# Kernel optimization log

Hardware: AMD Instinct MI355X
Metric: run time of the kernel (lower is better)

The kernel has to match this reference:

```python
import jax, jax.numpy as jnp
import numpy as np

N = 50000       # nodes
E = 800000      # directed edges
F_IN = 128      # input feature dim
HID = 128       # hidden channels
DEPTH = 3


def glorot(key, shape):
    lim = (6.0 / (shape[0] + shape[-1])) ** 0.5
    return jax.random.uniform(key, shape, jnp.float32, -lim, lim)


def setup_inputs():
    key = jax.random.key(0)
    ks = jax.random.split(key, 20)
    inp = {
        "x": jax.random.normal(ks[0], (N, F_IN), jnp.float32),
        "edge_index": jax.random.randint(ks[1], (E, 2), 0, N),
        "y": jax.random.randint(ks[2], (N,), 0, 2),
    }
    dd = [(F_IN, HID), (HID, HID), (HID, HID), (HID, HID)]
    for i, (a, b) in enumerate(dd):
        inp[f"Wd{i}"] = glorot(ks[3 + i], (a, b))
        inp[f"bd{i}"] = jnp.zeros((b,), jnp.float32)
    for i in range(DEPTH):
        inp[f"Wp{i}"] = glorot(ks[7 + i], (2 * HID,))
        inp[f"bp{i}"] = jnp.zeros((), jnp.float32)
    du = [(2 * HID, HID), (2 * HID, HID), (2 * HID + F_IN, 1)]
    for i, (a, b) in enumerate(du):
        inp[f"Wu{i}"] = glorot(ks[10 + i], (a, b))
        inp[f"bu{i}"] = jnp.zeros((b,), jnp.float32)
    return inp


def gcn_conv(x, src, dst, ew, W, b):
    """GCNConv(improved=True): A_hat = A + 2I, symmetric normalization.
    ew masks invalid (deduped/padded) edges with 0."""
    n = x.shape[0]
    deg = 2.0 + jax.ops.segment_sum(ew, dst, num_segments=n)  # self-loop weight 2
    dinv = jax.lax.rsqrt(deg)
    xw = x @ W                                   # [n, out]
    norm = ew * dinv[src] * dinv[dst]            # [E]
    out = jax.ops.segment_sum(xw[src] * norm[:, None], dst, num_segments=n)
    out = out + (2.0 * dinv * dinv)[:, None] * xw  # self-loop contribution
    return out + b


def connected_components(src, dst, sel, n):
    """Weak CC over selected edges via min-label propagation + pointer jumping.
    Returns per-node label = min node index in its component."""
    s = jnp.where(sel, src, 0)  # masked edges become (0,0) self-loops
    d = jnp.where(sel, dst, 0)

    def body(state):
        lab, _ = state
        m = jnp.minimum(lab[s], lab[d])
        new = lab.at[s].min(m).at[d].min(m)
        new = new[new]
        new = new[new]
        return new, jnp.any(new != lab)

    lab, _ = jax.lax.while_loop(lambda st: st[1], body,
                                (jnp.arange(n), jnp.array(True)))
    return lab


def cluster_pool(x, src, dst, ew, Wp, bp):
    """ClusterPooling (eval mode): score edges, contract score>0.5 edges,
    merge components (sum of members scaled by mean intra-cluster edge score).
    Pooled graph keeps N slots; cluster ids are representative node indices."""
    n, hid = x.shape
    valid = (ew > 0) & (src != dst)
    s = jax.nn.sigmoid(x[src] @ Wp[:hid] + x[dst] @ Wp[hid:] + bp)  # [E]
    sel = valid & (s > 0.5)
    cluster = jax.lax.stop_gradient(connected_components(src, dst, sel, n))
    csrc = cluster[src]
    ssum = jax.ops.segment_sum(jnp.where(sel, s, 0.0), csrc, num_segments=n)
    scnt = jax.ops.segment_sum(sel.astype(x.dtype), csrc, num_segments=n)
    w = jnp.where(scnt > 0, ssum / jnp.maximum(scnt, 1.0), 1.0)  # singletons -> 1
    new_x = jax.ops.segment_sum(x, cluster, num_segments=n) * w[:, None]
    # remap edges to clusters, drop self-loops, coalesce duplicates (static shape)
    a = jnp.where(valid, cluster[src], n)
    b = jnp.where(valid, cluster[dst], n)
    loop = a == b
    a = jnp.where(loop, n, a)
    b = jnp.where(loop, n, b)
    order = jnp.lexsort((b, a))
    a, b = a[order], b[order]
    dup = jnp.concatenate([jnp.zeros((1,), bool),
                           (a[1:] == a[:-1]) & (b[1:] == b[:-1])])
    keep = (a < n) & (~dup)
    new_ew = keep.astype(x.dtype)
    a = jnp.where(keep, a, 0)
    b = jnp.where(keep, b, 0)
    return new_x, a, b, new_ew, (src, dst, ew, cluster)


def reference(x, edge_index, y,
              Wd0, bd0, Wd1, bd1, Wd2, bd2, Wd3, bd3,
              Wp0, bp0, Wp1, bp1, Wp2, bp2,
              Wu0, bu0, Wu1, bu1, Wu2, bu2):
    Wd = [Wd0, Wd1, Wd2, Wd3]; bd = [bd0, bd1, bd2, bd3]
    Wp = [Wp0, Wp1, Wp2]; bp = [bp0, bp1, bp2]
    Wu = [Wu0, Wu1, Wu2]; bu = [bu0, bu1, bu2]
    src = edge_index[:, 0]
    dst = edge_index[:, 1]
    ew = jnp.ones(src.shape[0], x.dtype)
    x_in = x
    memory, infos = [], []
    for i in range(DEPTH):
        x = jax.nn.relu(gcn_conv(x, src, dst, ew, Wd[i], bd[i]))
        memory.append(x)
        x, src, dst, ew, info = cluster_pool(x, src, dst, ew, Wp[i], bp[i])
        infos.append(info)
    memory[0] = jnp.concatenate([memory[0], x_in], axis=-1)
    x = gcn_conv(x, src, dst, ew, Wd[3], bd[3])
    for i in range(DEPTH):
        src, dst, ew, cluster = infos.pop()
        x = x[cluster]                                  # unpool
        x = jnp.concatenate([memory.pop(), x], axis=-1)  # skip connection
        x = gcn_conv(x, src, dst, ew, Wu[i], bu[i])
        if i < DEPTH - 1:
            x = jax.nn.relu(x)
    return jax.nn.sigmoid(x).ravel()
```

## Files before the change

### kernel.cpp

```cpp
#include <hip/hip_runtime.h>
#include <math.h>

#define NN 50000
#define EE 800000
#define HID 128
#define HSZ (1u<<21)
#define CC_ROUNDS 8
#define GN 196
#define WH 512
#define CH 128


static __device__ __forceinline__ float sigmoid_ref(float t) {
  if (t >= 0.f) { float e = expf(-t); return 1.f / (1.f + e); }
  float e = expf(t); return e / (1.f + e);
}

static __device__ __forceinline__ int edge_count(const int* cntp, int cnst) {
  return cntp ? *cntp : cnst;
}


__global__ void k_split_edges(const int* __restrict__ ei, int* __restrict__ s, int* __restrict__ d) {
  int T = gridDim.x*blockDim.x;
  for (int e = blockIdx.x*blockDim.x+threadIdx.x; e < EE; e += T) {
    s[e] = ei[2*e]; d[e] = ei[2*e+1];
  }
}

__global__ void k_degree(const int* __restrict__ eB, const int* cntp, int cnst, int* __restrict__ deg) {
  int n = edge_count(cntp, cnst);
  int T = gridDim.x*blockDim.x;
  for (int e = blockIdx.x*blockDim.x+threadIdx.x; e < n; e += T)
    atomicAdd(&deg[eB[e]], 1);
}

__global__ void k_scan1(const int* __restrict__ deg, int* __restrict__ rp, int* __restrict__ bsum) {
  __shared__ int sh[256];
  int tid = threadIdx.x; int i = blockIdx.x*256 + tid;
  int v = (i < NN) ? deg[i] : 0;
  sh[tid] = v; __syncthreads();
  for (int off = 1; off < 256; off <<= 1) {
    int t = (tid >= off) ? sh[tid-off] : 0;
    __syncthreads(); sh[tid] += t; __syncthreads();
  }
  if (i < NN) rp[i] = sh[tid] - v;
  if (tid == 255) bsum[blockIdx.x] = sh[255];
}

__global__ void k_scan2(int* __restrict__ bsum, int* __restrict__ rp, int nb) {
  __shared__ int sh[256];
  int tid = threadIdx.x;
  int v = (tid < nb) ? bsum[tid] : 0;
  sh[tid] = v; __syncthreads();
  for (int off = 1; off < 256; off <<= 1) {
    int t = (tid >= off) ? sh[tid-off] : 0;
    __syncthreads(); sh[tid] += t; __syncthreads();
  }
  if (tid < nb) bsum[tid] = sh[tid] - v;
  if (tid == 255) rp[NN] = sh[255];
}

__global__ void k_scan3(int* __restrict__ rp, const int* __restrict__ bsum, int* __restrict__ cursor,
                        const int* __restrict__ deg, float* __restrict__ dinv) {
  int i = blockIdx.x*256 + threadIdx.x;
  if (i < NN) {
    int r = rp[i] + bsum[blockIdx.x];
    rp[i] = r; cursor[i] = r;
    if (dinv) dinv[i] = (float)(1.0 / sqrt((double)(deg[i] + 2)));
  }
}

__global__ void k_csrfill(const int* __restrict__ eA, const int* __restrict__ eB,
                          const int* cntp, int cnst,
                          int* __restrict__ cursor, int* __restrict__ csr, int* __restrict__ dstE) {
  int n = edge_count(cntp, cnst);
  int T = gridDim.x*blockDim.x;
  for (int e = blockIdx.x*blockDim.x+threadIdx.x; e < n; e += T) {
    int d = eB[e];
    int p = atomicAdd(&cursor[d], 1);
    csr[p] = eA[e];
    dstE[p] = d;
  }
}


__global__ __launch_bounds__(256) void k_matmul(
    const float* __restrict__ A0, const int* __restrict__ idx0, int reluA0,
    const float* __restrict__ rsA, const float* __restrict__ rcA,
    const float* __restrict__ A1, const int* __restrict__ idx1, int reluA1,
    int K, const float* __restrict__ W, const float* __restrict__ dinv,
    const float* __restrict__ bias, float* __restrict__ xs, float* __restrict__ outi)
{
  __shared__ __align__(16) float As[64][68];
  __shared__ __align__(16) float Bs[64][HID];
  const int tid  = threadIdx.x;
  const int row0 = blockIdx.x * 64;
  const int colg = (tid & 31) * 4;
  const int rowg = (tid >> 5) * 8;
  float acc[8][4];
  #pragma unroll
  for (int i = 0; i < 8; ++i) { acc[i][0]=0.f; acc[i][1]=0.f; acc[i][2]=0.f; acc[i][3]=0.f; }

  for (int kc = 0; kc < K; kc += 64) {
    const bool first = (kc < 128);
    const float* Asrc = first ? A0 : A1;
    const int*   aidx = first ? idx0 : idx1;
    const int    relu = first ? reluA0 : reluA1;
    const int klocal  = first ? kc : (kc - 128);
    #pragma unroll
    for (int t = tid; t < 64*16; t += 256) {
      int r  = t >> 4;
      int k4 = (t & 15) << 2;
      int grow = row0 + r;
      if (grow >= NN) grow = NN - 1;
      int gr = aidx ? aidx[grow] : grow;
      float4 v = *(const float4*)(Asrc + (size_t)gr*HID + klocal + k4);
      if (relu) {
        v.x = fmaxf(v.x,0.f); v.y = fmaxf(v.y,0.f);
        v.z = fmaxf(v.z,0.f); v.w = fmaxf(v.w,0.f);
      }
      if (first && rsA) {
        float c = rcA[gr];
        float w = (c > 0.f) ? rsA[gr]/c : 1.f;
        v.x *= w; v.y *= w; v.z *= w; v.w *= w;
      }
      As[k4+0][r] = v.x; As[k4+1][r] = v.y; As[k4+2][r] = v.z; As[k4+3][r] = v.w;
    }
    #pragma unroll
    for (int t = tid; t < 64*32; t += 256) {
      int kk = t >> 5;
      int c4 = (t & 31) << 2;
      *(float4*)&Bs[kk][c4] = *(const float4*)(W + (size_t)(kc+kk)*HID + c4);
    }
    __syncthreads();
    #pragma unroll 8
    for (int k = 0; k < 64; ++k) {
      float4 a0 = *(const float4*)&As[k][rowg];
      float4 a1 = *(const float4*)&As[k][rowg+4];
      float4 b  = *(const float4*)&Bs[k][colg];
      float ar[8] = {a0.x,a0.y,a0.z,a0.w,a1.x,a1.y,a1.z,a1.w};
      #pragma unroll
      for (int i = 0; i < 8; ++i) {
        acc[i][0] += ar[i]*b.x; acc[i][1] += ar[i]*b.y;
        acc[i][2] += ar[i]*b.z; acc[i][3] += ar[i]*b.w;
      }
    }
    __syncthreads();
  }
  float4 bb = *(const float4*)(bias + colg);
  #pragma unroll
  for (int i = 0; i < 8; ++i) {
    int r = row0 + rowg + i;
    if (r < NN) {
      float dv = dinv[r];
      float4 xv = make_float4(acc[i][0]*dv, acc[i][1]*dv, acc[i][2]*dv, acc[i][3]*dv);
      *(float4*)(xs + (size_t)r*HID + colg) = xv;
      float c2 = 2.f*dv;
      *(float4*)(outi + (size_t)r*HID + colg) =
        make_float4(xv.x*c2+bb.x, xv.y*c2+bb.y, xv.z*c2+bb.z, xv.w*c2+bb.w);
    }
  }
}

__global__ __launch_bounds__(256) void k_edgeagg(
    const float* __restrict__ xs, const int* __restrict__ csr, const int* __restrict__ dstE,
    const float* __restrict__ dinv, float* __restrict__ out,
    const int* cntp, int cnst)
{
  __shared__ int sh_s[8][CH];
  __shared__ int sh_d[8][CH];
  int n = edge_count(cntp, cnst);
  const int lane = threadIdx.x & 31;
  const int gsub = threadIdx.x >> 5;
  const int grp  = blockIdx.x*8 + gsub;
  const int p0   = grp * CH;
  if (p0 >= n) return;
  const int cnt = min(CH, n - p0);

  for (int j = lane; j < cnt; j += 32) {
    sh_s[gsub][j] = csr[p0 + j];
    sh_d[gsub][j] = dstE[p0 + j];
  }

  float4 pf[4];
  #pragma unroll
  for (int j = 0; j < 4; ++j) {
    if (j < cnt) {
      int s = sh_s[gsub][j];
      pf[j] = *(const float4*)(xs + (size_t)s*HID + lane*4);
    }
  }

  int cur = sh_d[gsub][0];
  float4 acc = make_float4(0.f,0.f,0.f,0.f);
  int flushes = 0;

  #pragma unroll 4
  for (int i = 0; i < cnt; ++i) {
    float4 xv = pf[i & 3];
    int jn = i + 4;
    if (jn < cnt) {
      int sn = sh_s[gsub][jn];
      pf[i & 3] = *(const float4*)(xs + (size_t)sn*HID + lane*4);
    }
    int d = sh_d[gsub][i];
    if (d != cur) {
      float dv = dinv[cur];
      float* o = out + (size_t)cur*HID + lane*4;
      if (flushes == 0) {
        atomicAdd(o+0, acc.x*dv); atomicAdd(o+1, acc.y*dv);
        atomicAdd(o+2, acc.z*dv); atomicAdd(o+3, acc.w*dv);
      } else {
        float4 ov = *(float4*)o;
        ov.x += acc.x*dv; ov.y += acc.y*dv; ov.z += acc.z*dv; ov.w += acc.w*dv;
        *(float4*)o = ov;
      }
      ++flushes;
      acc = make_float4(0.f,0.f,0.f,0.f);
      cur = d;
    }
    acc.x += xv.x; acc.y += xv.y; acc.z += xv.z; acc.w += xv.w;
  }
  float dv = dinv[cur];
  float* o = out + (size_t)cur*HID + lane*4;
  atomicAdd(o+0, acc.x*dv); atomicAdd(o+1, acc.y*dv);
  atomicAdd(o+2, acc.z*dv); atomicAdd(o+3, acc.w*dv);
}


__global__ __launch_bounds__(256) void k_node_ab(
    const float* __restrict__ h, const float* __restrict__ Wp,
    float* __restrict__ an, float* __restrict__ bn)
{
  int l = threadIdx.x & 63;
  int sub = threadIdx.x >> 6;
  float w0 = Wp[l], w1 = Wp[64+l], w2 = Wp[128+l], w3 = Wp[192+l];
  for (int g = blockIdx.x; g*4 < NN; g += gridDim.x) {
    int v = g*4 + sub;
    if (v >= NN) continue;
    float h0 = fmaxf(h[(size_t)v*HID + l], 0.f);
    float h1 = fmaxf(h[(size_t)v*HID + 64 + l], 0.f);
    float a = h0*w0 + h1*w1;
    float b = h0*w2 + h1*w3;
    #pragma unroll
    for (int off = 32; off; off >>= 1) { a += __shfl_down(a, off); b += __shfl_down(b, off); }
    if (l == 0) { an[v] = a; bn[v] = b; }
  }
}

__global__ void k_labinit(int* __restrict__ lab, int* __restrict__ flags,
                          int* __restrict__ selcnt, int* ecnt_next,
                          float* __restrict__ ssum2) {
  int i = blockIdx.x*256 + threadIdx.x;
  int T = gridDim.x*256;
  if (i < NN) lab[i] = i;
  for (int j = i; j < 2*NN; j += T) ssum2[j] = 0.f;
  if (i < 32) flags[i] = 0;
  if (i == 32) *selcnt = 0;
  if (i == 33 && ecnt_next) *ecnt_next = 0;
}

__global__ __launch_bounds__(256) void k_score_sel(
    const int* __restrict__ eA, const int* __restrict__ eB, const int* cntp, int cnst,
    const float* __restrict__ an, const float* __restrict__ bn, const float* __restrict__ bp,
    int* __restrict__ selA, int* __restrict__ selB, float* __restrict__ selS,
    int* __restrict__ selcnt)
{
  int n = edge_count(cntp, cnst);
  int T = gridDim.x*blockDim.x;
  int lane = threadIdx.x & 63;
  for (int e = blockIdx.x*blockDim.x+threadIdx.x; e < n; e += T) {
    int a = eA[e], b = eB[e];
    bool pred = false; float s = 0.f;
    if (a != b) {
      s = sigmoid_ref(an[a] + bn[b] + bp[0]);
      pred = s > 0.5f;
    }
    unsigned long long mask = __ballot(pred);
    if (mask) {
      int leader = __ffsll((long long)mask) - 1;
      int total  = __popcll(mask);
      int base = 0;
      if (lane == leader) base = atomicAdd(selcnt, total);
      base = __shfl(base, leader);
      if (pred) {
        int off = __popcll(mask & ((1ull << lane) - 1));
        selA[base+off] = a; selB[base+off] = b; selS[base+off] = s;
      }
    }
  }
}

__global__ __launch_bounds__(256) void k_hook(
    const int* __restrict__ selA, const int* __restrict__ selB, const int* __restrict__ selcnt,
    int* __restrict__ lab, const int* flagPrev, int* __restrict__ flagCur)
{
  if (flagPrev && *flagPrev == 0) return;
  int n = *selcnt;
  int T = gridDim.x*blockDim.x;
  bool changed = false;
  for (int i = blockIdx.x*blockDim.x+threadIdx.x; i < n; i += T) {
    int a = selA[i], b = selB[i];
    int la = lab[a], lb = lab[b];
    if (la == lb) continue;
    int pla = lab[la], plb = lab[lb];
    int m = min(pla, plb);
    if (la > m && lab[a] > m) atomicMin(&lab[a], m);
    if (lb > m && lab[b] > m) atomicMin(&lab[b], m);
    if (pla > m) atomicMin(&lab[la], m);
    if (plb > m) atomicMin(&lab[lb], m);
    changed = true;
  }
  unsigned long long m2 = __ballot(changed);
  if (m2 && (threadIdx.x & 63) == __ffsll((long long)m2) - 1) *flagCur = 1;
}

__global__ void k_jump(int* __restrict__ lab, const int* flagPrev, int* __restrict__ flagCur) {
  if (flagPrev && *flagPrev == 0) return;
  int i = blockIdx.x*256 + threadIdx.x;
  bool changed = false;
  if (i < NN) {
    int l0 = lab[i];
    int l = lab[l0]; l = lab[l]; l = lab[l];
    if (l < l0) { lab[i] = l; changed = true; }
  }
  unsigned long long m2 = __ballot(changed);
  if (m2 && (threadIdx.x & 63) == __ffsll((long long)m2) - 1) *flagCur = 1;
}

__global__ __launch_bounds__(256) void k_wsum(
    const int* __restrict__ selA, const float* __restrict__ selS,
    const int* __restrict__ selcnt, const int* __restrict__ cl,
    float* __restrict__ ssum, float* __restrict__ scnt)
{
  __shared__ int key[WH];
  __shared__ float vs[WH];
  __shared__ float vc[WH];
  int n = *selcnt;
  for (int i = threadIdx.x; i < WH; i += 256) { key[i] = -1; vs[i] = 0.f; vc[i] = 0.f; }
  __syncthreads();
  int T = gridDim.x*blockDim.x;
  for (int e = blockIdx.x*blockDim.x+threadIdx.x; e < n; e += T) {
    int c = cl[selA[e]];
    float s = selS[e];
    unsigned h = ((unsigned)c * 2654435761u) & (WH-1);
    bool done = false;
    for (int probe = 0; probe < 32; ++probe) {
      int k = key[h];
      if (k == c) { atomicAdd(&vs[h], s); atomicAdd(&vc[h], 1.f); done = true; break; }
      if (k == -1) {
        int old = atomicCAS(&key[h], -1, c);
        if (old == -1 || old == c) { atomicAdd(&vs[h], s); atomicAdd(&vc[h], 1.f); done = true; break; }
      }
      h = (h+1) & (WH-1);
    }
    if (!done) { atomicAdd(&ssum[c], s); atomicAdd(&scnt[c], 1.f); }
  }
  __syncthreads();
  for (int i = threadIdx.x; i < WH; i += 256) {
    if (key[i] >= 0) { atomicAdd(&ssum[key[i]], vs[i]); atomicAdd(&scnt[key[i]], vc[i]); }
  }
}

__global__ __launch_bounds__(128) void k_poolsum(const float* __restrict__ h,
                                                 const int* __restrict__ cl, float* __restrict__ p) {
  int f = threadIdx.x;
  int base = blockIdx.x * 64;
  int cur = -1; float acc = 0.f;
  for (int j = 0; j < 64; ++j) {
    int v = base + j;
    if (v >= NN) break;
    int c = cl[v];
    float x = fmaxf(h[(size_t)v*HID + f], 0.f);
    if (c == cur) acc += x;
    else {
      if (cur >= 0) atomicAdd(&p[(size_t)cur*HID + f], acc);
      cur = c; acc = x;
    }
  }
  if (cur >= 0) atomicAdd(&p[(size_t)cur*HID + f], acc);
}

__global__ __launch_bounds__(256) void k_contract(
    const int* __restrict__ eA, const int* __restrict__ eB, const int* cntp, int cnst,
    const int* __restrict__ cl, unsigned long long* __restrict__ tab,
    int* __restrict__ outA, int* __restrict__ outB, int* __restrict__ ocnt, int lev)
{
  int n = edge_count(cntp, cnst);
  int T = gridDim.x*blockDim.x;
  int lane = threadIdx.x & 63;
  for (int e = blockIdx.x*blockDim.x+threadIdx.x; e < n; e += T) {
    int s = eA[e], d = eB[e];
    bool keep = false; int a = 0, b = 0;
    if (s != d) {
      a = cl[s]; b = cl[d];
      if (a != b) {
        unsigned long long key = ((unsigned long long)lev << 34) |
                                 ((unsigned long long)a << 17) | (unsigned long long)b;
        unsigned long long hh = key * 0x9E3779B97F4A7C15ull;
        unsigned idx = (unsigned)(hh >> 40) & (HSZ - 1);
        while (true) {
          unsigned long long prev = atomicCAS(&tab[idx], ~0ull, key);
          if (prev == ~0ull) { keep = true; break; }
          if (prev == key) break;
          idx = (idx + 1) & (HSZ - 1);
        }
      }
    }
    unsigned long long mask = __ballot(keep);
    if (mask) {
      int leader = __ffsll((long long)mask) - 1;
      int total  = __popcll(mask);
      int base = 0;
      if (lane == leader) base = atomicAdd(ocnt, total);
      base = __shfl(base, leader);
      if (keep) {
        int off = __popcll(mask & ((1ull << lane) - 1));
        outA[base+off] = a; outB[base+off] = b;
      }
    }
  }
}


__global__ __launch_bounds__(256) void k_matvec384(
    const float* __restrict__ h1, const float* __restrict__ xin,
    const float* __restrict__ u1, const int* __restrict__ cl0,
    const float* __restrict__ Wu2, float* __restrict__ zw)
{
  int l = threadIdx.x & 63;
  int sub = threadIdx.x >> 6;
  float w0 = Wu2[l],     w1 = Wu2[64+l],  w2 = Wu2[128+l];
  float w3 = Wu2[192+l], w4 = Wu2[256+l], w5 = Wu2[320+l];
  for (int g = blockIdx.x; g*4 < NN; g += gridDim.x) {
    int v = g*4 + sub;
    if (v >= NN) continue;
    int gg = cl0[v];
    float s = fmaxf(h1[(size_t)v*HID + l], 0.f)       * w0
            + fmaxf(h1[(size_t)v*HID + 64 + l], 0.f)  * w1
            + xin[(size_t)v*HID + l]                  * w2
            + xin[(size_t)v*HID + 64 + l]             * w3
            + fmaxf(u1[(size_t)gg*HID + l], 0.f)      * w4
            + fmaxf(u1[(size_t)gg*HID + 64 + l], 0.f) * w5;
    #pragma unroll
    for (int off = 32; off; off >>= 1) s += __shfl_down(s, off);
    if (l == 0) zw[v] = s;
  }
}

__global__ void k_final(const float* __restrict__ zw, const int* __restrict__ rp,
                        const int* __restrict__ csr, const float* __restrict__ dinv,
                        const float* __restrict__ bu, float* __restrict__ out) {
  int T = gridDim.x*blockDim.x;
  for (int v = blockIdx.x*blockDim.x+threadIdx.x; v < NN; v += T) {
    float acc = 0.f;
    int p0 = rp[v], p1 = rp[v+1];
    for (int p = p0; p < p1; ++p) { int s = csr[p]; acc += zw[s]*dinv[s]; }
    float dv = dinv[v];
    float t = acc*dv + 2.f*dv*dv*zw[v] + bu[0];
    out[v] = sigmoid_ref(t);
  }
}


extern "C" void kernel_launch(void* const* d_in, const int* in_sizes, int n_in,
                              void* d_out, int out_size, void* d_ws, size_t ws_size,
                              hipStream_t stream) {
  const float* x_in = (const float*)d_in[0];
  const int*   ei   = (const int*)d_in[1];
  const float* Wd0 = (const float*)d_in[3];  const float* bd0 = (const float*)d_in[4];
  const float* Wd1 = (const float*)d_in[5];  const float* bd1 = (const float*)d_in[6];
  const float* Wd2 = (const float*)d_in[7];  const float* bd2 = (const float*)d_in[8];
  const float* Wd3 = (const float*)d_in[9];  const float* bd3 = (const float*)d_in[10];
  const float* Wp0 = (const float*)d_in[11]; const float* bp0 = (const float*)d_in[12];
  const float* Wp1 = (const float*)d_in[13]; const float* bp1 = (const float*)d_in[14];
  const float* Wp2 = (const float*)d_in[15]; const float* bp2 = (const float*)d_in[16];
  const float* Wu0 = (const float*)d_in[17]; const float* bu0 = (const float*)d_in[18];
  const float* Wu1 = (const float*)d_in[19]; const float* bu1 = (const float*)d_in[20];
  const float* Wu2 = (const float*)d_in[21]; const float* bu2 = (const float*)d_in[22];
  float* out = (float*)d_out;
  (void)in_sizes; (void)n_in; (void)out_size;

  char* wp = (char*)d_ws;
  auto alloc = [&](size_t bytes) -> void* {
    void* p = (void*)wp;
    wp += (bytes + 255) & ~(size_t)255;
    return p;
  };
  float* B[6]; for (int i = 0; i < 6; ++i) B[i] = (float*)alloc((size_t)NN*HID*4);
  int *eA[4], *eB[4];
  for (int i = 0; i < 4; ++i) { eA[i] = (int*)alloc((size_t)EE*4); eB[i] = (int*)alloc((size_t)EE*4); }
  int* cl[3];      for (int i = 0; i < 3; ++i) cl[i]    = (int*)alloc((size_t)NN*4);
  float* dinvL[4]; for (int i = 0; i < 4; ++i) dinvL[i] = (float*)alloc((size_t)NN*4);
  int* rpL[4]; int* csrL[4]; int* dstL[4];
  for (int i = 0; i < 4; ++i) {
    rpL[i]  = (int*)alloc((size_t)(NN+1)*4);
    csrL[i] = (int*)alloc((size_t)EE*4);
    dstL[i] = (int*)alloc((size_t)EE*4);
  }
  int*   selA = (int*)alloc((size_t)EE*4);
  int*   selB = (int*)alloc((size_t)EE*4);
  float* selS = (float*)alloc((size_t)EE*4);
  int* deg    = (int*)alloc((size_t)NN*4);
  int* cursor = (int*)alloc((size_t)NN*4);
  int* bsum   = (int*)alloc(256*4);
  float* an   = (float*)alloc((size_t)NN*4);
  float* bn   = (float*)alloc((size_t)NN*4);
  float* ssum = (float*)alloc((size_t)2*NN*4);
  float* scnt = ssum + NN;
  float* zw   = (float*)alloc((size_t)NN*4);
  int* selcnt = (int*)alloc(256);
  int* ecnt   = (int*)alloc(256);
  int* flags  = (int*)alloc(256);
  unsigned long long* tab = (unsigned long long*)alloc((size_t)HSZ*8);
  if ((size_t)(wp - (char*)d_ws) > ws_size) return;

  k_split_edges<<<1024,256,0,stream>>>(ei, eA[0], eB[0]);
  hipMemsetAsync(tab, 0xFF, (size_t)HSZ*8, stream);

  auto cntp = [&](int lev) -> const int* { return lev ? (ecnt + lev) : nullptr; };

  auto build_level = [&](int lev) {
    hipMemsetAsync(deg, 0, (size_t)NN*4, stream);
    k_degree<<<512,256,0,stream>>>(eB[lev], cntp(lev), EE, deg);
    k_scan1<<<GN,256,0,stream>>>(deg, rpL[lev], bsum);
    k_scan2<<<1,256,0,stream>>>(bsum, rpL[lev], GN);
    k_scan3<<<GN,256,0,stream>>>(rpL[lev], bsum, cursor, deg, dinvL[lev]);
    k_csrfill<<<512,256,0,stream>>>(eA[lev], eB[lev], cntp(lev), EE, cursor, csrL[lev], dstL[lev]);
  };

  const int GAGG = (EE + 8*CH - 1) / (8*CH);
  auto do_conv = [&](const float* A0, int reluA0, const float* rs, const float* rc,
                     const float* A1, const int* i1, int reluA1, int K,
                     const float* W, const float* bias, int lev, float* xs, float* outp) {
    k_matmul<<<(NN+63)/64,256,0,stream>>>(A0, nullptr, reluA0, rs, rc,
                                          A1, i1, reluA1, K, W, dinvL[lev], bias, xs, outp);
    k_edgeagg<<<GAGG,256,0,stream>>>(xs, csrL[lev], dstL[lev], dinvL[lev], outp, cntp(lev), EE);
  };

  auto do_pool = [&](const float* h, int lev, int ci, float* p, const float* Wp, const float* bp) {
    k_node_ab<<<512,256,0,stream>>>(h, Wp, an, bn);
    k_labinit<<<GN,256,0,stream>>>(cl[ci], flags, selcnt, ecnt + lev + 1, ssum);
    k_score_sel<<<512,256,0,stream>>>(eA[lev], eB[lev], cntp(lev), EE, an, bn, bp,
                                      selA, selB, selS, selcnt);
    for (int r = 0; r < CC_ROUNDS; ++r) {
      const int* fp = r ? (flags + r - 1) : nullptr;
      k_hook<<<512,256,0,stream>>>(selA, selB, selcnt, cl[ci], fp, flags + r);
      k_jump<<<GN,256,0,stream>>>(cl[ci], fp, flags + r);
    }
    k_wsum<<<64,256,0,stream>>>(selA, selS, selcnt, cl[ci], ssum, scnt);
    hipMemsetAsync(p, 0, (size_t)NN*HID*4, stream);
    k_poolsum<<<(NN+63)/64,128,0,stream>>>(h, cl[ci], p);
    k_contract<<<512,256,0,stream>>>(eA[lev], eB[lev], cntp(lev), EE, cl[ci], tab,
                                     eA[lev+1], eB[lev+1], ecnt + lev + 1, lev);
  };

  build_level(0);
  do_conv(x_in, 0, nullptr, nullptr, nullptr, nullptr, 0, 128, Wd0, bd0, 0, B[5], B[0]);
  do_pool(B[0], 0, 0, B[3], Wp0, bp0);
  build_level(1);
  do_conv(B[3], 0, ssum, scnt, nullptr, nullptr, 0, 128, Wd1, bd1, 1, B[5], B[1]);
  do_pool(B[1], 1, 1, B[3], Wp1, bp1);
  build_level(2);
  do_conv(B[3], 0, ssum, scnt, nullptr, nullptr, 0, 128, Wd2, bd2, 2, B[5], B[2]);
  do_pool(B[2], 2, 2, B[3], Wp2, bp2);
  build_level(3);
  do_conv(B[3], 0, ssum, scnt, nullptr, nullptr, 0, 128, Wd3, bd3, 3, B[5], B[4]);
  do_conv(B[2], 1, nullptr, nullptr, B[4], cl[2], 0, 256, Wu0, bu0, 2, B[5], B[3]);
  do_conv(B[1], 1, nullptr, nullptr, B[3], cl[1], 1, 256, Wu1, bu1, 1, B[5], B[4]);
  k_matvec384<<<512,256,0,stream>>>(B[0], x_in, B[4], cl[0], Wu2, zw);
  k_final<<<512,256,0,stream>>>(zw, rpL[0], csrL[0], dinvL[0], bu2, out);
}
```

Measured before the change: 1.631 ms.

## Deepen edge-aggregation gather prefetch and fuse CC hook with pointer jumping

The edge-aggregation kernel now keeps eight row gathers in flight instead of four, to hide more gather latency. The connected-components hook and pointer-jump kernels are merged into one kernel per round, halving the launches in the CC loop. Inside the fused kernel, jumping runs without a grid-wide barrier after hooking. Jumps can therefore read labels that are only partly hooked. This is tolerated because min-label propagation is monotone, but it may change how many rounds are needed to converge within CC_ROUNDS. The larger prefetch buffer raises register use.

```diff
diff --git a/kernel.cpp b/kernel.cpp
--- a/kernel.cpp
+++ b/kernel.cpp
@@ -9,6 +9,7 @@
 #define GN 196
 #define WH 512
 #define CH 128
+#define PF 8
 
 
 static __device__ __forceinline__ float sigmoid_ref(float t) {
@@ -183,9 +184,9 @@
     sh_d[gsub][j] = dstE[p0 + j];
   }
 
-  float4 pf[4];
+  float4 pf[PF];
   #pragma unroll
-  for (int j = 0; j < 4; ++j) {
+  for (int j = 0; j < PF; ++j) {
     if (j < cnt) {
       int s = sh_s[gsub][j];
       pf[j] = *(const float4*)(xs + (size_t)s*HID + lane*4);
@@ -196,13 +197,13 @@
   float4 acc = make_float4(0.f,0.f,0.f,0.f);
   int flushes = 0;
 
-  #pragma unroll 4
+  #pragma unroll 8
   for (int i = 0; i < cnt; ++i) {
-    float4 xv = pf[i & 3];
-    int jn = i + 4;
+    float4 xv = pf[i & (PF-1)];
+    int jn = i + PF;
     if (jn < cnt) {
       int sn = sh_s[gsub][jn];
-      pf[i & 3] = *(const float4*)(xs + (size_t)sn*HID + lane*4);
+      pf[i & (PF-1)] = *(const float4*)(xs + (size_t)sn*HID + lane*4);
     }
     int d = sh_d[gsub][i];
     if (d != cur) {
@@ -292,15 +293,16 @@
   }
 }
 
-__global__ __launch_bounds__(256) void k_hook(
+__global__ __launch_bounds__(256) void k_ccround(
     const int* __restrict__ selA, const int* __restrict__ selB, const int* __restrict__ selcnt,
     int* __restrict__ lab, const int* flagPrev, int* __restrict__ flagCur)
 {
   if (flagPrev && *flagPrev == 0) return;
   int n = *selcnt;
   int T = gridDim.x*blockDim.x;
+  int t0 = blockIdx.x*blockDim.x+threadIdx.x;
   bool changed = false;
-  for (int i = blockIdx.x*blockDim.x+threadIdx.x; i < n; i += T) {
+  for (int i = t0; i < n; i += T) {
     int a = selA[i], b = selB[i];
     int la = lab[a], lb = lab[b];
     if (la == lb) continue;
@@ -312,18 +314,10 @@
     if (plb > m) atomicMin(&lab[lb], m);
     changed = true;
   }
-  unsigned long long m2 = __ballot(changed);
-  if (m2 && (threadIdx.x & 63) == __ffsll((long long)m2) - 1) *flagCur = 1;
-}
-
-__global__ void k_jump(int* __restrict__ lab, const int* flagPrev, int* __restrict__ flagCur) {
-  if (flagPrev && *flagPrev == 0) return;
-  int i = blockIdx.x*256 + threadIdx.x;
-  bool changed = false;
-  if (i < NN) {
-    int l0 = lab[i];
+  for (int v = t0; v < NN; v += T) {
+    int l0 = lab[v];
     int l = lab[l0]; l = lab[l]; l = lab[l];
-    if (l < l0) { lab[i] = l; changed = true; }
+    if (l < l0) { lab[v] = l; changed = true; }
   }
   unsigned long long m2 = __ballot(changed);
   if (m2 && (threadIdx.x & 63) == __ffsll((long long)m2) - 1) *flagCur = 1;
@@ -546,8 +540,7 @@
                                       selA, selB, selS, selcnt);
     for (int r = 0; r < CC_ROUNDS; ++r) {
       const int* fp = r ? (flags + r - 1) : nullptr;
-      k_hook<<<512,256,0,stream>>>(selA, selB, selcnt, cl[ci], fp, flags + r);
-      k_jump<<<GN,256,0,stream>>>(cl[ci], fp, flags + r);
+      k_ccround<<<512,256,0,stream>>>(selA, selB, selcnt, cl[ci], fp, flags + r);
     }
     k_wsum<<<64,256,0,stream>>>(selA, selS, selcnt, cl[ci], ssum, scnt);
     hipMemsetAsync(p, 0, (size_t)NN*HID*4, stream);
```

Result: no change. 1.653 ms (+1.4%).
